# Kernel optimization log

Hardware: AMD Instinct MI355X
Metric: run time of the kernel (lower is better)

The kernel has to match this reference:

```python
import jax, jax.numpy as jnp
import numpy as np

N_EMBD = 1024
N_HEAD = 16
HEAD_DIM = N_EMBD // N_HEAD


def setup_inputs() -> dict:
    key = jax.random.key(0)
    k1, k2, k3, k4, k5 = jax.random.split(key, 5)
    x = jax.random.normal(k1, (4, 2048, N_EMBD), dtype=jnp.float32)
    s = 1.0 / np.sqrt(N_EMBD)
    W_attn = jax.random.normal(k2, (N_EMBD, 3 * N_EMBD), dtype=jnp.float32) * s
    b_attn = jnp.zeros((3 * N_EMBD,), dtype=jnp.float32)
    W_proj = jax.random.normal(k3, (N_EMBD, N_EMBD), dtype=jnp.float32) * s
    b_proj = jnp.zeros((N_EMBD,), dtype=jnp.float32)
    return {"x": x, "W_attn": W_attn, "b_attn": b_attn, "W_proj": W_proj, "b_proj": b_proj}


def _attention(x, W_attn, b_attn, W_proj, b_proj):
    B, T, C = x.shape
    qkv = jnp.einsum("btc,cd->btd", x, W_attn) + b_attn  # [B,T,3C]
    q, k, v = jnp.split(qkv, 3, axis=-1)
    # [B,T,C] -> [B,H,T,D]
    def heads(t):
        return t.reshape(B, T, N_HEAD, HEAD_DIM).transpose(0, 2, 1, 3)
    q, k, v = heads(q), heads(k), heads(v)
    scale = 1.0 / np.sqrt(HEAD_DIM)
    scores = jnp.einsum("bhqd,bhkd->bhqk", q, k) * scale  # [B,H,T,T]
    causal = jnp.tril(jnp.ones((T, T), dtype=bool))
    scores = jnp.where(causal, scores, jnp.finfo(scores.dtype).min)
    attn = jax.nn.softmax(scores, axis=-1)
    y = jnp.einsum("bhqk,bhkd->bhqd", attn, v)  # [B,H,T,D]
    y = y.transpose(0, 2, 1, 3).reshape(B, T, C)
    return jnp.einsum("btc,cd->btd", y, W_proj) + b_proj


def reference(x, W_attn, b_attn, W_proj, b_proj):
    return _attention(x, W_attn, b_attn, W_proj, b_proj)
```

## Files before the change

### kernel.cpp

```cpp
#include <hip/hip_runtime.h>
#include <hip/hip_bf16.h>

#define BB 4
#define TT 2048
#define CC 1024
#define HH 16
#define DD 64
#define BT (BB*TT)
#define C3 (3*CC)
#define LDST 72
#define QSCALE 0.18033688011112042f

typedef __attribute__((ext_vector_type(8))) short short8;
typedef __attribute__((ext_vector_type(4))) float f32x4;

__device__ __forceinline__ short f2bs(float f) {
  __hip_bfloat16 h = __float2bfloat16(f);
  return *reinterpret_cast<short*>(&h);
}

__device__ __forceinline__ void gl_lds16(const short* g, short* l) {
  __builtin_amdgcn_global_load_lds(
      (const __attribute__((address_space(1))) void*)(g),
      (__attribute__((address_space(3))) void*)(l), 16, 0, 0);
}

__global__ __launch_bounds__(256)
void prep(const float* __restrict__ Wa, short* __restrict__ Wat,
          const float* __restrict__ Wp, short* __restrict__ Wpt,
          const float* __restrict__ x, short* __restrict__ Xb)
{
  __shared__ float Lt[64][65];
  const int bx = blockIdx.x;
  if (bx >= 64) {
    size_t chunk = (size_t)(bx - 64) * 16 + blockIdx.y;
    size_t i = (chunk * 256 + threadIdx.x) * 8;
    float4 a = *reinterpret_cast<const float4*>(x + i);
    float4 b = *reinterpret_cast<const float4*>(x + i + 4);
    short8 o;
    o[0] = f2bs(a.x); o[1] = f2bs(a.y); o[2] = f2bs(a.z); o[3] = f2bs(a.w);
    o[4] = f2bs(b.x); o[5] = f2bs(b.y); o[6] = f2bs(b.z); o[7] = f2bs(b.w);
    *reinterpret_cast<short8*>(Xb + i) = o;
    return;
  }
  const bool isA = (bx < 48);
  const float* in  = isA ? Wa  : Wp;
  short*       out = isA ? Wat : Wpt;
  const int N  = isA ? C3 : CC;
  const int n0 = (isA ? bx : bx - 48) * 64;
  const int k0 = blockIdx.y * 64;
  const int cx = threadIdx.x & 15, rr = threadIdx.x >> 4;
#pragma unroll
  for (int p = 0; p < 4; ++p) {
    int kr = p * 16 + rr;
    float4 u = *reinterpret_cast<const float4*>(in + (size_t)(k0 + kr) * N + n0 + cx * 4);
    Lt[kr][cx * 4 + 0] = u.x;
    Lt[kr][cx * 4 + 1] = u.y;
    Lt[kr][cx * 4 + 2] = u.z;
    Lt[kr][cx * 4 + 3] = u.w;
  }
  __syncthreads();
#pragma unroll
  for (int p = 0; p < 4; ++p) {
    int nr = p * 16 + rr;
    short4 o;
    o.x = f2bs(Lt[cx * 4 + 0][nr]);
    o.y = f2bs(Lt[cx * 4 + 1][nr]);
    o.z = f2bs(Lt[cx * 4 + 2][nr]);
    o.w = f2bs(Lt[cx * 4 + 3][nr]);
    *reinterpret_cast<short4*>(out + (size_t)(n0 + nr) * CC + k0 + cx * 4) = o;
  }
}

template<bool QKV>
__global__ __launch_bounds__(512, 2)
void gemm256(const short* __restrict__ A, const short* __restrict__ Bt,
             const float* __restrict__ bias,
             short* __restrict__ qb, short* __restrict__ kb, short* __restrict__ vb,
             float* __restrict__ out)
{
  __shared__ __align__(16) short As[2][2 * 256 * 32];
  __shared__ __align__(16) short Bs[2][2 * 256 * 32];

  const int t = threadIdx.x;
  const int lane = t & 63;
  const int l16 = lane & 15, quad = lane >> 4;
  const int w = t >> 6;
  const int wr = w >> 2, wc = w & 3;

  const int per   = gridDim.x >> 3;
  const int chunk = (blockIdx.x & 7) * per + (blockIdx.x >> 3);
  const int NBC   = QKV ? 12 : 4;
  const int brow  = chunk / NBC, bcol = chunk % NBC;
  const int row0  = brow * 256;
  const int col0  = bcol * 256;

  auto stageQ = [&](int bufS, int kcS, int tileS, bool isA) {
#pragma unroll
    for (int l = 0; l < 2; ++l) {
      int gq = l * 512 + t;
      int rq = gq >> 2;
      int g  = (gq & 3) ^ ((rq >> 1) & 3);
      if (isA) {
        gl_lds16(A + (size_t)(row0 + rq) * CC + tileS * 64 + kcS * 32 + g * 8,
                 &As[bufS][kcS * 8192 + gq * 8]);
      } else {
        gl_lds16(Bt + (size_t)(col0 + rq) * CC + tileS * 64 + kcS * 32 + g * 8,
                 &Bs[bufS][kcS * 8192 + gq * 8]);
      }
    }
  };

  f32x4 acc[8][4];
#pragma unroll
  for (int i = 0; i < 8; ++i)
#pragma unroll
    for (int j = 0; j < 4; ++j) acc[i][j] = (f32x4){0.f, 0.f, 0.f, 0.f};

  stageQ(0, 0, 0, true);  stageQ(0, 0, 0, false);
  stageQ(0, 1, 0, true);  stageQ(0, 1, 0, false);
  stageQ(1, 0, 1, true);  stageQ(1, 0, 1, false);
  asm volatile("s_waitcnt vmcnt(8)" ::: "memory");
  __builtin_amdgcn_s_barrier();

#pragma unroll
  for (int u = 0; u < 16; ++u) {
    const int cb = u & 1;
    const short* Ac = As[cb];
    const short* Bc = Bs[cb];
    short8 bf[4];
#pragma unroll
    for (int ph = 0; ph < 4; ++ph) {
      const int kc = ph >> 1, q = ph & 1;

      if (q == 0) {
#pragma unroll
        for (int j = 0; j < 4; ++j) {
          int rb = wc * 64 + j * 16 + l16;
          bf[j] = *reinterpret_cast<const short8*>(
              &Bc[kc * 8192 + rb * 32 + (((quad ^ (rb >> 1)) & 3) << 3)]);
        }
      }
      short8 af[4];
#pragma unroll
      for (int iq = 0; iq < 4; ++iq) {
        int ra = wr * 128 + (q * 4 + iq) * 16 + l16;
        af[iq] = *reinterpret_cast<const short8*>(
            &Ac[kc * 8192 + ra * 32 + (((quad ^ (ra >> 1)) & 3) << 3)]);
      }

      if      (ph == 0) { if (u < 15) stageQ((u + 1) & 1, 1, u + 1, true ); }
      else if (ph == 1) { if (u < 15) stageQ((u + 1) & 1, 1, u + 1, false); }
      else if (ph == 2) { if (u < 14) stageQ(u & 1,       0, u + 2, true ); }
      else              { if (u < 14) stageQ(u & 1,       0, u + 2, false); }

      __builtin_amdgcn_s_barrier();
      asm volatile("s_waitcnt lgkmcnt(0)" ::: "memory");
      __builtin_amdgcn_sched_barrier(0);

      __builtin_amdgcn_s_setprio(1);
#pragma unroll
      for (int iq = 0; iq < 4; ++iq)
#pragma unroll
        for (int j = 0; j < 4; ++j)
          acc[q * 4 + iq][j] =
              __builtin_amdgcn_mfma_f32_16x16x32_bf16(af[iq], bf[j], acc[q * 4 + iq][j], 0, 0, 0);
      __builtin_amdgcn_s_setprio(0);

      if (ph == 1) {
        if (u == 15)      { asm volatile("s_waitcnt vmcnt(0)" ::: "memory"); }
        else              { asm volatile("s_waitcnt vmcnt(8)" ::: "memory"); }
      } else if (ph == 3) {
        if (u < 14)       { asm volatile("s_waitcnt vmcnt(8)" ::: "memory"); }
        else if (u == 14) { asm volatile("s_waitcnt vmcnt(4)" ::: "memory"); }
      }
      __builtin_amdgcn_s_barrier();
    }
  }

  if constexpr (QKV) {
#pragma unroll
    for (int j = 0; j < 4; ++j) {
      int colb = col0 + wc * 64 + j * 16 + l16;
      int sel  = colb >> 10, cin = colb & 1023;
      int h    = cin >> 6,  dd  = cin & 63;
      float bv = bias[colb];
#pragma unroll
      for (int i = 0; i < 8; ++i)
#pragma unroll
        for (int r = 0; r < 4; ++r) {
          int row = row0 + wr * 128 + i * 16 + quad * 4 + r;
          int bi = row >> 11, tt = row & 2047;
          float val = acc[i][j][r] + bv;
          size_t hb = (size_t)(bi * HH + h);
          if (sel == 0) {
            qb[(hb * TT + tt) * DD + dd] = f2bs(val * QSCALE);
          } else if (sel == 1) {
            kb[(hb * TT + tt) * DD + dd] = f2bs(val);
          } else {
            int tp = (tt & ~63) | (((tt & 15) << 2) | ((tt >> 4) & 3));
            vb[(hb * DD + dd) * TT + tp] = f2bs(val);
          }
        }
    }
  } else {
#pragma unroll
    for (int j = 0; j < 4; ++j) {
      int col = col0 + wc * 64 + j * 16 + l16;
      float bv = bias[col];
#pragma unroll
      for (int i = 0; i < 8; ++i)
#pragma unroll
        for (int r = 0; r < 4; ++r) {
          int row = row0 + wr * 128 + i * 16 + quad * 4 + r;
          out[(size_t)row * CC + col] = acc[i][j][r] + bv;
        }
    }
  }
}

__global__ __launch_bounds__(256, 4)
void attn_mfma(const short* __restrict__ Qb, const short* __restrict__ Kb,
               const short* __restrict__ Vb, short* __restrict__ Y)
{
  __shared__ __align__(16) short Ks[64 * LDST];
  __shared__ __align__(16) short Vt[64 * LDST];
  __shared__ __align__(16) short Pw[4 * 16 * LDST];

  const int t    = threadIdx.x;
  const int w    = t >> 6;
  const int lane = t & 63;
  const int l16  = lane & 15;
  const int quad = lane >> 4;

  const int linear = blockIdx.x + 16 * (blockIdx.y + 16 * blockIdx.z);
  const int nb  = (linear & 7) * 128 + (linear >> 3);
  const int qt0 = nb & 15;
  const int h   = (nb >> 4) & 15;
  const int bi  = nb >> 8;
  const size_t head = (size_t)(bi * HH + h) * TT * DD;

  short* myP = &Pw[w * 16 * LDST];
  const int sr = t >> 2;
  const int sc = (t & 3) << 4;

  const int qts[2] = { qt0, 31 - qt0 };

#pragma unroll
  for (int half = 0; half < 2; ++half) {
    const int qt = qts[half];
    const int q0 = qt * 64;

    short8 qf[2];
#pragma unroll
    for (int kc = 0; kc < 2; ++kc)
      qf[kc] = *reinterpret_cast<const short8*>(
          &Qb[head + (size_t)(q0 + w * 16 + l16) * DD + kc * 32 + quad * 8]);

    f32x4 O[4];
#pragma unroll
    for (int dt = 0; dt < 4; ++dt) O[dt] = (f32x4){0.f, 0.f, 0.f, 0.f};
    float lsum[4] = {};

    for (int kt = 0; kt <= qt; ++kt) {
      const int k0 = kt * 64;
      __syncthreads();

      {
        const short* kg = Kb + head + (size_t)(k0 + sr) * DD + sc;
        short8 a = *reinterpret_cast<const short8*>(kg);
        short8 b = *reinterpret_cast<const short8*>(kg + 8);
        *reinterpret_cast<short8*>(&Ks[sr * LDST + sc])     = a;
        *reinterpret_cast<short8*>(&Ks[sr * LDST + sc + 8]) = b;
        const short* vg = Vb + head + (size_t)sr * TT + k0 + sc;
        short8 c = *reinterpret_cast<const short8*>(vg);
        short8 d = *reinterpret_cast<const short8*>(vg + 8);
        *reinterpret_cast<short8*>(&Vt[sr * LDST + sc])     = c;
        *reinterpret_cast<short8*>(&Vt[sr * LDST + sc + 8]) = d;
      }
      __syncthreads();

      short8 kf[4][2];
#pragma unroll
      for (int nt = 0; nt < 4; ++nt)
#pragma unroll
        for (int kc = 0; kc < 2; ++kc)
          kf[nt][kc] = *reinterpret_cast<const short8*>(
              &Ks[(nt * 16 + l16) * LDST + kc * 32 + quad * 8]);

      f32x4 s[4];
#pragma unroll
      for (int nt = 0; nt < 4; ++nt) s[nt] = (f32x4){0.f, 0.f, 0.f, 0.f};
      __builtin_amdgcn_s_setprio(1);
#pragma unroll
      for (int nt = 0; nt < 4; ++nt)
#pragma unroll
        for (int kc = 0; kc < 2; ++kc)
          s[nt] = __builtin_amdgcn_mfma_f32_16x16x32_bf16(qf[kc], kf[nt][kc], s[nt], 0, 0, 0);
      __builtin_amdgcn_s_setprio(0);

      const int rowg_base = q0 + w * 16 + quad * 4;
#pragma unroll
      for (int r = 0; r < 4; ++r) {
        const int rowg = rowg_base + r;
        short pk[4];
#pragma unroll
        for (int nt = 0; nt < 4; ++nt) {
          float e = (k0 + nt * 16 + l16 <= rowg) ? __builtin_amdgcn_exp2f(s[nt][r]) : 0.f;
          lsum[r] += e;
          pk[nt] = f2bs(e);
        }
        short4 p4; p4.x = pk[0]; p4.y = pk[1]; p4.z = pk[2]; p4.w = pk[3];
        *reinterpret_cast<short4*>(&myP[(quad * 4 + r) * LDST + (l16 << 2)]) = p4;
      }

      __builtin_amdgcn_s_setprio(1);
#pragma unroll
      for (int cc = 0; cc < 2; ++cc) {
        short8 pf = *reinterpret_cast<const short8*>(
            &myP[l16 * LDST + cc * 32 + quad * 8]);
#pragma unroll
        for (int dt = 0; dt < 4; ++dt) {
          short8 vf = *reinterpret_cast<const short8*>(
              &Vt[(dt * 16 + l16) * LDST + cc * 32 + quad * 8]);
          O[dt] = __builtin_amdgcn_mfma_f32_16x16x32_bf16(pf, vf, O[dt], 0, 0, 0);
        }
      }
      __builtin_amdgcn_s_setprio(0);
    }

    float linv[4];
#pragma unroll
    for (int r = 0; r < 4; ++r) {
      float s = lsum[r];
      s += __shfl_xor(s, 1);
      s += __shfl_xor(s, 2);
      s += __shfl_xor(s, 4);
      s += __shfl_xor(s, 8);
      linv[r] = 1.f / s;
    }
#pragma unroll
    for (int dt = 0; dt < 4; ++dt)
#pragma unroll
      for (int r = 0; r < 4; ++r) {
        int tg = q0 + w * 16 + quad * 4 + r;
        Y[((size_t)bi * TT + tg) * CC + h * DD + dt * 16 + l16] =
            f2bs(O[dt][r] * linv[r]);
      }
  }
}

extern "C" void kernel_launch(void* const* d_in, const int* in_sizes, int n_in,
                              void* d_out, int out_size, void* d_ws, size_t ws_size,
                              hipStream_t stream) {
  const float* x  = (const float*)d_in[0];
  const float* Wa = (const float*)d_in[1];
  const float* ba = (const float*)d_in[2];
  const float* Wp = (const float*)d_in[3];
  const float* bp = (const float*)d_in[4];
  float* out = (float*)d_out;

  const size_t NELT = (size_t)BB * HH * TT * DD;
  short* qb  = (short*)d_ws;
  short* kb  = qb + NELT;
  short* vb  = kb + NELT;
  short* Xb  = vb + NELT;
  short* Wat = Xb  + (size_t)BT * CC;
  short* Wpt = Wat + (size_t)CC * C3;
  short* Yb  = Wpt + (size_t)CC * CC;

  prep<<<dim3(64 + 256, 16), 256, 0, stream>>>(Wa, Wat, Wp, Wpt, x, Xb);

  gemm256<true> <<<dim3((C3 / 256) * (BT / 256)), 512, 0, stream>>>(Xb, Wat, ba, qb, kb, vb, nullptr);
  attn_mfma     <<<dim3(16, HH, BB),              256, 0, stream>>>(qb, kb, vb, Yb);
  gemm256<false><<<dim3((CC / 256) * (BT / 256)), 512, 0, stream>>>(Yb, Wpt, bp, nullptr, nullptr, nullptr, out);
}
```

Baseline: 283.8 us.

## Stage QKV epilogue through LDS for vectorized 16-byte global stores

The QKV GEMM epilogue now writes bf16 results into a unified shared buffer, transposed for V, in two half-tile passes. It then issues coalesced short8 stores to the head-major q/k/v layouts, replacing the scattered 2-byte per-element stores. The main loop is also restructured into a non-fully-unrolled loop of an always-inline k-tile lambda, which reduces code size but may change scheduling. The extra syncthreads and LDS round trip add some epilogue latency.

New measurement: 270.2 us. 1.05x faster.

```diff
diff --git a/kernel.cpp b/kernel.cpp
--- a/kernel.cpp
+++ b/kernel.cpp
@@ -79,8 +79,7 @@
              short* __restrict__ qb, short* __restrict__ kb, short* __restrict__ vb,
              float* __restrict__ out)
 {
-  __shared__ __align__(16) short As[2][2 * 256 * 32];
-  __shared__ __align__(16) short Bs[2][2 * 256 * 32];
+  __shared__ __align__(16) short SMEM[65536];
 
   const int t = threadIdx.x;
   const int lane = t & 63;
@@ -95,7 +94,7 @@
   const int row0  = brow * 256;
   const int col0  = bcol * 256;
 
-  auto stageQ = [&](int bufS, int kcS, int tileS, bool isA) {
+  auto stageQ = [&](int bufS, int kcS, int tileS, bool isA) __attribute__((always_inline)) {
 #pragma unroll
     for (int l = 0; l < 2; ++l) {
       int gq = l * 512 + t;
@@ -103,10 +102,10 @@
       int g  = (gq & 3) ^ ((rq >> 1) & 3);
       if (isA) {
         gl_lds16(A + (size_t)(row0 + rq) * CC + tileS * 64 + kcS * 32 + g * 8,
-                 &As[bufS][kcS * 8192 + gq * 8]);
+                 &SMEM[bufS * 16384 + kcS * 8192 + gq * 8]);
       } else {
         gl_lds16(Bt + (size_t)(col0 + rq) * CC + tileS * 64 + kcS * 32 + g * 8,
-                 &Bs[bufS][kcS * 8192 + gq * 8]);
+                 &SMEM[32768 + bufS * 16384 + kcS * 8192 + gq * 8]);
       }
     }
   };
@@ -116,6 +115,58 @@
   for (int i = 0; i < 8; ++i)
 #pragma unroll
     for (int j = 0; j < 4; ++j) acc[i][j] = (f32x4){0.f, 0.f, 0.f, 0.f};
+
+  auto kTile = [&](int u, int cb, int tm) __attribute__((always_inline)) {
+    const short* Ac = &SMEM[cb * 16384];
+    const short* Bc = &SMEM[32768 + cb * 16384];
+    short8 bf[4];
+#pragma unroll
+    for (int ph = 0; ph < 4; ++ph) {
+      const int kc = ph >> 1, q = ph & 1;
+      if (q == 0) {
+#pragma unroll
+        for (int j = 0; j < 4; ++j) {
+          int rb = wc * 64 + j * 16 + l16;
+          bf[j] = *reinterpret_cast<const short8*>(
+              &Bc[kc * 8192 + rb * 32 + (((quad ^ (rb >> 1)) & 3) << 3)]);
+        }
+      }
+      short8 af[4];
+#pragma unroll
+      for (int iq = 0; iq < 4; ++iq) {
+        int ra = wr * 128 + (q * 4 + iq) * 16 + l16;
+        af[iq] = *reinterpret_cast<const short8*>(
+            &Ac[kc * 8192 + ra * 32 + (((quad ^ (ra >> 1)) & 3) << 3)]);
+      }
+
+      if      (ph == 0) { if (tm < 2) stageQ(cb ^ 1, 1, u + 1, true ); }
+      else if (ph == 1) { if (tm < 2) stageQ(cb ^ 1, 1, u + 1, false); }
+      else if (ph == 2) { if (tm < 1) stageQ(cb,     0, u + 2, true ); }
+      else              { if (tm < 1) stageQ(cb,     0, u + 2, false); }
+
+      __builtin_amdgcn_s_barrier();
+      asm volatile("s_waitcnt lgkmcnt(0)" ::: "memory");
+      __builtin_amdgcn_sched_barrier(0);
+
+      __builtin_amdgcn_s_setprio(1);
+#pragma unroll
+      for (int iq = 0; iq < 4; ++iq)
+#pragma unroll
+        for (int j = 0; j < 4; ++j)
+          acc[q * 4 + iq][j] =
+              __builtin_amdgcn_mfma_f32_16x16x32_bf16(af[iq], bf[j], acc[q * 4 + iq][j], 0, 0, 0);
+      __builtin_amdgcn_s_setprio(0);
+
+      if (ph == 1) {
+        if (tm == 2) { asm volatile("s_waitcnt vmcnt(0)" ::: "memory"); }
+        else         { asm volatile("s_waitcnt vmcnt(8)" ::: "memory"); }
+      } else if (ph == 3) {
+        if      (tm == 0) { asm volatile("s_waitcnt vmcnt(8)" ::: "memory"); }
+        else if (tm == 1) { asm volatile("s_waitcnt vmcnt(4)" ::: "memory"); }
+      }
+      __builtin_amdgcn_s_barrier();
+    }
+  };
 
   stageQ(0, 0, 0, true);  stageQ(0, 0, 0, false);
   stageQ(0, 1, 0, true);  stageQ(0, 1, 0, false);
@@ -123,85 +174,69 @@
   asm volatile("s_waitcnt vmcnt(8)" ::: "memory");
   __builtin_amdgcn_s_barrier();
 
-#pragma unroll
-  for (int u = 0; u < 16; ++u) {
-    const int cb = u & 1;
-    const short* Ac = As[cb];
-    const short* Bc = Bs[cb];
-    short8 bf[4];
-#pragma unroll
-    for (int ph = 0; ph < 4; ++ph) {
-      const int kc = ph >> 1, q = ph & 1;
-
-      if (q == 0) {
+  for (int u = 0; u < 14; u += 2) {
+    kTile(u,     0, 0);
+    kTile(u + 1, 1, 0);
+  }
+  kTile(14, 0, 1);
+  kTile(15, 1, 2);
+
+  if constexpr (QKV) {
+    const int sel = col0 >> 10;
+#pragma unroll
+    for (int hp = 0; hp < 2; ++hp) {
+      __syncthreads();
+      if (wr == hp) {
 #pragma unroll
         for (int j = 0; j < 4; ++j) {
-          int rb = wc * 64 + j * 16 + l16;
-          bf[j] = *reinterpret_cast<const short8*>(
-              &Bc[kc * 8192 + rb * 32 + (((quad ^ (rb >> 1)) & 3) << 3)]);
-        }
-      }
-      short8 af[4];
-#pragma unroll
-      for (int iq = 0; iq < 4; ++iq) {
-        int ra = wr * 128 + (q * 4 + iq) * 16 + l16;
-        af[iq] = *reinterpret_cast<const short8*>(
-            &Ac[kc * 8192 + ra * 32 + (((quad ^ (ra >> 1)) & 3) << 3)]);
-      }
-
-      if      (ph == 0) { if (u < 15) stageQ((u + 1) & 1, 1, u + 1, true ); }
-      else if (ph == 1) { if (u < 15) stageQ((u + 1) & 1, 1, u + 1, false); }
-      else if (ph == 2) { if (u < 14) stageQ(u & 1,       0, u + 2, true ); }
-      else              { if (u < 14) stageQ(u & 1,       0, u + 2, false); }
-
-      __builtin_amdgcn_s_barrier();
-      asm volatile("s_waitcnt lgkmcnt(0)" ::: "memory");
-      __builtin_amdgcn_sched_barrier(0);
-
-      __builtin_amdgcn_s_setprio(1);
-#pragma unroll
-      for (int iq = 0; iq < 4; ++iq)
-#pragma unroll
-        for (int j = 0; j < 4; ++j)
-          acc[q * 4 + iq][j] =
-              __builtin_amdgcn_mfma_f32_16x16x32_bf16(af[iq], bf[j], acc[q * 4 + iq][j], 0, 0, 0);
-      __builtin_amdgcn_s_setprio(0);
-
-      if (ph == 1) {
-        if (u == 15)      { asm volatile("s_waitcnt vmcnt(0)" ::: "memory"); }
-        else              { asm volatile("s_waitcnt vmcnt(8)" ::: "memory"); }
-      } else if (ph == 3) {
-        if (u < 14)       { asm volatile("s_waitcnt vmcnt(8)" ::: "memory"); }
-        else if (u == 14) { asm volatile("s_waitcnt vmcnt(4)" ::: "memory"); }
-      }
-      __builtin_amdgcn_s_barrier();
-    }
-  }
-
-  if constexpr (QKV) {
-#pragma unroll
-    for (int j = 0; j < 4; ++j) {
-      int colb = col0 + wc * 64 + j * 16 + l16;
-      int sel  = colb >> 10, cin = colb & 1023;
-      int h    = cin >> 6,  dd  = cin & 63;
-      float bv = bias[colb];
-#pragma unroll
-      for (int i = 0; i < 8; ++i)
-#pragma unroll
-        for (int r = 0; r < 4; ++r) {
-          int row = row0 + wr * 128 + i * 16 + quad * 4 + r;
-          int bi = row >> 11, tt = row & 2047;
-          float val = acc[i][j][r] + bv;
-          size_t hb = (size_t)(bi * HH + h);
-          if (sel == 0) {
-            qb[(hb * TT + tt) * DD + dd] = f2bs(val * QSCALE);
-          } else if (sel == 1) {
-            kb[(hb * TT + tt) * DD + dd] = f2bs(val);
-          } else {
-            int tp = (tt & ~63) | (((tt & 15) << 2) | ((tt >> 4) & 3));
-            vb[(hb * DD + dd) * TT + tp] = f2bs(val);
-          }
-        }
+          const int colL = wc * 64 + j * 16 + l16;
+          const float bv = bias[col0 + colL];
+#pragma unroll
+          for (int i = 0; i < 8; ++i)
+#pragma unroll
+            for (int r = 0; r < 4; ++r) {
+              const int rl = i * 16 + quad * 4 + r;
+              float val = acc[i][j][r] + bv;
+              if (sel == 0) val *= QSCALE;
+              short vs = f2bs(val);
+              if (sel == 2) {
+                int tpl = (rl & ~63) | ((rl & 15) << 2) | ((rl >> 4) & 3);
+                SMEM[colL * 136 + tpl] = vs;
+              } else {
+                SMEM[rl * 264 + colL] = vs;
+              }
+            }
+        }
+      }
+      __syncthreads();
+      const int Rbase = row0 + hp * 128;
+      const int bi = Rbase >> 11;
+      if (sel != 2) {
+        short* __restrict__ dstB = (sel == 0) ? qb : kb;
+#pragma unroll
+        for (int rep = 0; rep < 8; ++rep) {
+          int slot = rep * 512 + t;
+          int rl = slot >> 5, ch = slot & 31;
+          short8 vv = *reinterpret_cast<const short8*>(&SMEM[rl * 264 + ch * 8]);
+          int tt  = (Rbase & 2047) + rl;
+          int cin = (col0 + ch * 8) & 1023;
+          int h = cin >> 6, dd = cin & 63;
+          *reinterpret_cast<short8*>(
+              &dstB[(((size_t)(bi * HH + h)) * TT + tt) * DD + dd]) = vv;
+        }
+      } else {
+#pragma unroll
+        for (int rep = 0; rep < 8; ++rep) {
+          int slot = rep * 512 + t;
+          int dcol = slot >> 4, ch = slot & 15;
+          short8 vv = *reinterpret_cast<const short8*>(&SMEM[dcol * 136 + ch * 8]);
+          int cin = (col0 + dcol) & 1023;
+          int h = cin >> 6, dd = cin & 63;
+          int ttb = (Rbase & 2047) + ch * 8;
+          *reinterpret_cast<short8*>(
+              &vb[(((size_t)(bi * HH + h)) * DD + dd) * TT + ttb]) = vv;
+        }
+      }
     }
   } else {
 #pragma unroll
```
